# Kernel optimization log

Hardware: AMD Instinct MI355X
Metric: run time of the kernel (lower is better)

## Reference

```python
import jax, jax.numpy as jnp
import numpy as np

D = 1024

def setup_inputs() -> dict:
    key = jax.random.key(0)
    ks = jax.random.split(key, 9)
    s = 1.0 / np.sqrt(D)
    x = jax.random.normal(ks[0], (8, 4096, D), dtype=jnp.float32)
    Wq = jax.random.uniform(ks[1], (D, D), jnp.float32, -s, s)
    bq = jax.random.uniform(ks[2], (D,), jnp.float32, -s, s)
    Wk = jax.random.uniform(ks[3], (D, D), jnp.float32, -s, s)
    bk = jax.random.uniform(ks[4], (D,), jnp.float32, -s, s)
    Wv = jax.random.uniform(ks[5], (D, D), jnp.float32, -s, s)
    bv = jax.random.uniform(ks[6], (D,), jnp.float32, -s, s)
    Wo = jax.random.uniform(ks[7], (D, D), jnp.float32, -s, s)
    bo = jax.random.uniform(ks[8], (D,), jnp.float32, -s, s)
    return {"x": x, "Wq": Wq, "bq": bq, "Wk": Wk, "bk": bk,
            "Wv": Wv, "bv": bv, "Wo": Wo, "bo": bo}

def reference(x, Wq, bq, Wk, bk, Wv, bv, Wo, bo):
    # Linear projections (torch Linear: x @ W.T + b)
    Q = x @ Wq.T + bq
    K = x @ Wk.T + bk
    V = x @ Wv.T + bv
    # elu+1 feature map (positive features)
    Q = jax.nn.elu(Q) + 1.0
    K = jax.nn.elu(K) + 1.0
    # KV outer-product accumulation over sequence: [b, d, e]
    KV = jnp.einsum('bnd,bne->bde', K, V)
    # normalizer Z: [b, n]
    Z = jnp.einsum('bnd,bd->bn', Q, K.sum(axis=1) + 1e-6)
    context = jnp.einsum('bnd,bde->bne', Q, KV) / Z[..., None]
    return context @ Wo.T + bo
```

## Files before the change

kernel.cpp:

```cpp
#include <hip/hip_runtime.h>
#include <stdint.h>

typedef unsigned short u16;
typedef __attribute__((ext_vector_type(8))) short short8;
typedef __attribute__((ext_vector_type(4))) float f32x4;

#define SEQ    4096
#define NB     8
#define DMODEL 1024
#define MTOT   (NB*SEQ)

static __device__ __forceinline__ float bf2f(u16 u){
  union { float f; uint32_t i; } v; v.i = ((uint32_t)u) << 16; return v.f;
}
static __device__ __forceinline__ u16 f2bf(float f){
  union { float f; uint32_t i; } v; v.f = f;
  uint32_t i = v.i + 0x7FFFu + ((v.i >> 16) & 1u);
  return (u16)(i >> 16);
}

static __device__ __forceinline__ void stage16(const void* g, void* l){
  __builtin_amdgcn_global_load_lds(
      (const __attribute__((address_space(1))) void*)g,
      (__attribute__((address_space(3))) void*)l,
      16, 0, 0);
}

__global__ void cvt_f32_bf16(const float* __restrict__ s, u16* __restrict__ d, int n){
  int i = (blockIdx.x * 256 + threadIdx.x) * 8;
  if (i >= n) return;
  float4 a = *(const float4*)(s + i);
  float4 b = *(const float4*)(s + i + 4);
  union { u16 h[8]; short8 v; } o;
  o.h[0]=f2bf(a.x); o.h[1]=f2bf(a.y); o.h[2]=f2bf(a.z); o.h[3]=f2bf(a.w);
  o.h[4]=f2bf(b.x); o.h[5]=f2bf(b.y); o.h[6]=f2bf(b.z); o.h[7]=f2bf(b.w);
  *(short8*)(d + i) = o.v;
}

__global__ __launch_bounds__(256)
void cvt_tr(const float* __restrict__ in, u16* __restrict__ outN,
            u16* __restrict__ outT, int R, int C)
{
  __shared__ float t[64][65];
  const int tid = threadIdx.x;
  const int ntc = C >> 6;
  const int tr = blockIdx.x / ntc, tc = blockIdx.x % ntc;
  const int r0 = tr << 6, c0 = tc << 6;
  const int lrow = tid >> 4, lc4 = (tid & 15) << 2;
  #pragma unroll
  for (int p = 0; p < 4; p++){
    float4 v = *(const float4*)(in + (size_t)(r0 + p*16 + lrow) * C + c0 + lc4);
    t[p*16 + lrow][lc4+0] = v.x; t[p*16 + lrow][lc4+1] = v.y;
    t[p*16 + lrow][lc4+2] = v.z; t[p*16 + lrow][lc4+3] = v.w;
  }
  __syncthreads();
  const int wrow = tid >> 3, wc8 = (tid & 7) << 3;
  if (outN){
    #pragma unroll
    for (int p = 0; p < 2; p++){
      int r = p*32 + wrow;
      union { u16 h[8]; short8 v; } o;
      #pragma unroll
      for (int j = 0; j < 8; j++) o.h[j] = f2bf(t[r][wc8 + j]);
      *(short8*)(outN + (size_t)(r0 + r) * C + c0 + wc8) = o.v;
    }
  }
  #pragma unroll
  for (int p = 0; p < 2; p++){
    int c = p*32 + wrow;
    union { u16 h[8]; short8 v; } o;
    #pragma unroll
    for (int j = 0; j < 8; j++) o.h[j] = f2bf(t[wc8 + j][c]);
    *(short8*)(outT + (size_t)(c0 + c) * R + r0 + wc8) = o.v;
  }
}

__global__ void bo2_kernel(const float* __restrict__ Wo, const float* __restrict__ bv,
                           const float* __restrict__ bo, float* __restrict__ bo2){
  int o = blockIdx.x * 4 + (threadIdx.x >> 6);
  int lane = threadIdx.x & 63;
  const float* row = Wo + (size_t)o * DMODEL;
  float s = 0.f;
  #pragma unroll
  for (int j = 0; j < 4; j++){
    float4 w = *(const float4*)(row + j*256 + lane*4);
    float4 b = *(const float4*)(bv  + j*256 + lane*4);
    s += w.x*b.x + w.y*b.y + w.z*b.z + w.w*b.w;
  }
  for (int off = 32; off; off >>= 1) s += __shfl_xor(s, off);
  if (lane == 0) bo2[o] = bo[o] + s;
}

__global__ void ksum_kernel(const u16* __restrict__ Kt, float* __restrict__ Ksum){
  int wid  = blockIdx.x * 4 + (threadIdx.x >> 6);
  int lane = threadIdx.x & 63;
  int d = wid & 1023, b = wid >> 10;
  const u16* row = Kt + (size_t)d * MTOT + (size_t)b * SEQ;
  float s = 0.f;
  #pragma unroll
  for (int j = 0; j < 8; j++){
    short8 v = *(const short8*)(row + j * 512 + lane * 8);
    #pragma unroll
    for (int t = 0; t < 8; t++) s += bf2f((u16)v[t]);
  }
  for (int off = 32; off; off >>= 1) s += __shfl_xor(s, off);
  if (lane == 0) Ksum[wid] = s + 1e-6f;
}

__global__ void z_kernel(const u16* __restrict__ Qb, const float* __restrict__ Ksum,
                         float* __restrict__ Z){
  int n    = blockIdx.x * 4 + (threadIdx.x >> 6);
  int lane = threadIdx.x & 63;
  const u16*   qrow = Qb + (size_t)n * DMODEL;
  const float* ks   = Ksum + (size_t)(n >> 12) * DMODEL;
  float s = 0.f;
  #pragma unroll
  for (int j = 0; j < 2; j++){
    int base = j * 512 + lane * 8;
    short8 q  = *(const short8*)(qrow + base);
    float4 k0 = *(const float4*)(ks + base);
    float4 k1 = *(const float4*)(ks + base + 4);
    s += bf2f((u16)q[0])*k0.x + bf2f((u16)q[1])*k0.y + bf2f((u16)q[2])*k0.z + bf2f((u16)q[3])*k0.w
       + bf2f((u16)q[4])*k1.x + bf2f((u16)q[5])*k1.y + bf2f((u16)q[6])*k1.z + bf2f((u16)q[7])*k1.w;
  }
  for (int off = 32; off; off >>= 1) s += __shfl_xor(s, off);
  if (lane == 0) Z[n] = s;
}

__global__ __launch_bounds__(256)
void gemm_bt(const u16* __restrict__ A, int ldA,
             const u16* __restrict__ BT, int ldBT, int Kdim,
             u16* __restrict__ Obf, int ldO)
{
  __shared__ u16 Al[128 * 32];
  __shared__ u16 Bl[128 * 32];
  const int tid  = threadIdx.x;
  const int lane = tid & 63;
  const int w    = tid >> 6;
  const int tcol = blockIdx.x;
  const int trow = blockIdx.y;

  const u16* Ap = A  + (size_t)trow * 128 * ldA;
  const u16* Bp = BT + (size_t)tcol * 128 * ldBT;

  f32x4 acc[4][4] = {};
  const int srow = (lane >> 2);
  const int scol = (lane & 3) * 8;

  for (int k0 = 0; k0 < Kdim; k0 += 32){
    #pragma unroll
    for (int i = 0; i < 2; i++){
      int r = w * 32 + i * 16 + srow;
      stage16(Ap + (size_t)r * ldA  + k0 + scol, (char*)Al + w * 2048 + i * 1024);
      stage16(Bp + (size_t)r * ldBT + k0 + scol, (char*)Bl + w * 2048 + i * 1024);
    }
    __syncthreads();
    const int mr = (w >> 1) * 64, nc = (w & 1) * 64;
    const int lr = lane & 15, lk = (lane >> 4) * 8;
    short8 av[4], bv[4];
    #pragma unroll
    for (int mi = 0; mi < 4; mi++) av[mi] = *(const short8*)&Al[(mr + mi*16 + lr)*32 + lk];
    #pragma unroll
    for (int nj = 0; nj < 4; nj++) bv[nj] = *(const short8*)&Bl[(nc + nj*16 + lr)*32 + lk];
    #pragma unroll
    for (int mi = 0; mi < 4; mi++)
      #pragma unroll
      for (int nj = 0; nj < 4; nj++)
        acc[mi][nj] = __builtin_amdgcn_mfma_f32_16x16x32_bf16(av[mi], bv[nj], acc[mi][nj], 0, 0, 0);
    __syncthreads();
  }

  const int mr = (w >> 1) * 64, nc = (w & 1) * 64;
  const int lr = lane & 15, lq = lane >> 4;
  #pragma unroll
  for (int mi = 0; mi < 4; mi++)
    #pragma unroll
    for (int r = 0; r < 4; r++){
      const size_t grow = (size_t)trow * 128 + mr + mi * 16 + lq * 4 + r;
      #pragma unroll
      for (int nj = 0; nj < 4; nj++){
        const size_t gcol = (size_t)tcol * 128 + nc + nj * 16 + lr;
        Obf[grow * ldO + gcol] = f2bf(acc[mi][nj][r]);
      }
    }
}

static __device__ __forceinline__ void stage_chunk(
    const u16* __restrict__ g, int ld, int k0, u16* smem, int baseU16, int tid){
  #pragma unroll
  for (int c = 0; c < 2; c++){
    int lin = c * 512 + tid;
    int row = lin >> 3;
    int slotL = (lin & 7) ^ (row & 7);
    stage16(g + (size_t)row * ld + k0 + slotL * 8,
            (char*)smem + baseU16 * 2 + (c * 8 + (tid >> 6)) * 1024);
  }
}

template<int EPI>
__global__ __launch_bounds__(512, 2)
void gemm8(const u16* __restrict__ A, int ldA,
           const u16* __restrict__ BT, int ldBT, int NT,
           const float* __restrict__ bias, const float* __restrict__ Zv,
           u16* __restrict__ Obf, float* __restrict__ Of32, int ldO)
{
  __shared__ u16 smem[65536];
  const int tid  = threadIdx.x;
  const int lane = tid & 63;
  const int w    = tid >> 6;
  const int wm   = w >> 2, wn = w & 3;
  const int lr   = lane & 15, kq = lane >> 4;

  const int nwg  = gridDim.x;
  const int orig = blockIdx.x;
  const int work = (orig & 7) * (nwg >> 3) + (orig >> 3);
  int trow, tcol; size_t boff = 0;
  if (EPI == 1)      { trow = work & 3; tcol = work >> 2; }
  else               { tcol = work & 3; trow = work >> 2;
                       if (EPI == 2) boff = (size_t)(trow >> 4) * 1024; }
  const int tileM = trow * 256, tileN = tcol * 256;

  const u16* Ag = A + (size_t)tileM * ldA;
  const u16* Bg = BT + boff + (size_t)tileN * ldBT;

  f32x4 acc[8][4] = {};

#define STAGE(buf, k0) do { \
    stage_chunk(Ag,                    ldA,  (k0), smem, (buf) + 0,     tid); \
    stage_chunk(Ag + (size_t)128*ldA,  ldA,  (k0), smem, (buf) + 8192,  tid); \
    stage_chunk(Bg,                    ldBT, (k0), smem, (buf) + 16384, tid); \
    stage_chunk(Bg + (size_t)128*ldBT, ldBT, (k0), smem, (buf) + 24576, tid); \
  } while(0)

#define LDSA(MF, KC) (*(const short8*)(smem + cb + (wm*128 + (MF)*16 + lr)*64 + ((((KC)*4 + kq) ^ (lr & 7)) * 8)))
#define LDSB(NF, KC) (*(const short8*)(smem + cb + 16384 + (wn*64 + (NF)*16 + lr)*64 + ((((KC)*4 + kq) ^ (lr & 7)) * 8)))

  STAGE(0, 0);
  STAGE(32768, 64);
  asm volatile("s_waitcnt vmcnt(8)" ::: "memory");
  __builtin_amdgcn_sched_barrier(0);
  __builtin_amdgcn_s_barrier();

  for (int t = 0; t < NT; t++){
    const int cb = (t & 1) << 15;
    short8 af[4][2], ah[4][2], bf[4][2];
    #pragma unroll
    for (int i = 0; i < 4; i++){ af[i][0] = LDSA(i, 0);   af[i][1] = LDSA(i, 1); }
    #pragma unroll
    for (int i = 0; i < 4; i++){ bf[i][0] = LDSB(i, 0);   bf[i][1] = LDSB(i, 1); }
    __builtin_amdgcn_s_setprio(1);
    #pragma unroll
    for (int mi = 0; mi < 4; mi++)
      #pragma unroll
      for (int nj = 0; nj < 4; nj++)
        #pragma unroll
        for (int kc = 0; kc < 2; kc++)
          acc[mi][nj] = __builtin_amdgcn_mfma_f32_16x16x32_bf16(
              af[mi][kc], bf[nj][kc], acc[mi][nj], 0, 0, 0);
    __builtin_amdgcn_s_setprio(0);
    #pragma unroll
    for (int i = 0; i < 4; i++){ ah[i][0] = LDSA(4+i, 0); ah[i][1] = LDSA(4+i, 1); }
    __builtin_amdgcn_s_setprio(1);
    #pragma unroll
    for (int mi = 0; mi < 4; mi++)
      #pragma unroll
      for (int nj = 0; nj < 4; nj++)
        #pragma unroll
        for (int kc = 0; kc < 2; kc++)
          acc[4+mi][nj] = __builtin_amdgcn_mfma_f32_16x16x32_bf16(
              ah[mi][kc], bf[nj][kc], acc[4+mi][nj], 0, 0, 0);
    __builtin_amdgcn_s_setprio(0);

    __builtin_amdgcn_sched_barrier(0);
    __builtin_amdgcn_s_barrier();
    const int kNN = (t + 2 < NT ? t + 2 : NT - 1) * 64;
    STAGE(cb, kNN);
    asm volatile("s_waitcnt vmcnt(8)" ::: "memory");
    __builtin_amdgcn_sched_barrier(0);
    __builtin_amdgcn_s_barrier();
  }

#undef STAGE
#undef LDSA
#undef LDSB

  #pragma unroll
  for (int mf = 0; mf < 8; mf++){
    #pragma unroll
    for (int r = 0; r < 4; r++){
      const int grow = tileM + wm*128 + mf*16 + kq*4 + r;
      float rowB = 0.f, zin = 0.f;
      if (EPI == 1) rowB = bias[grow];
      if (EPI == 2) zin = 1.f / Zv[grow];
      #pragma unroll
      for (int nf = 0; nf < 4; nf++){
        const int gcol = tileN + wn*64 + nf*16 + lr;
        float v = acc[mf][nf][r];
        if (EPI == 0) { v += bias[gcol]; v = (v > 0.f) ? v + 1.f : __expf(v); }
        if (EPI == 1) { v += rowB;       v = (v > 0.f) ? v + 1.f : __expf(v); }
        if constexpr (EPI == 2) Of32[(size_t)grow * ldO + gcol] = v * zin + bias[gcol];
        else                    Obf [(size_t)grow * ldO + gcol] = f2bf(v);
      }
    }
  }
}

template<int EPI>
__global__ __launch_bounds__(512, 2)
void gemm8h(const u16* __restrict__ A, int ldA,
            const u16* __restrict__ BT, int ldBT, int NT,
            u16* __restrict__ Obf, int ldO)
{
  __shared__ u16 smem[49152];
  const int tid  = threadIdx.x;
  const int lane = tid & 63;
  const int w    = tid >> 6;
  const int wm   = w >> 2, wn = w & 3;
  const int lr   = lane & 15, kq = lane >> 4;

  const int orig = blockIdx.x;
  const int work = (orig & 7) * 32 + (orig >> 3);
  int trow, tcol; size_t aoff = 0, boff = 0, ooff = 0;
  if (EPI == 3) { int zb = work >> 5, sub = work & 31;
                  trow = sub & 7; tcol = sub >> 3;
                  aoff = (size_t)zb * SEQ; boff = aoff; ooff = (size_t)zb << 20; }
  else          { trow = work & 7; tcol = work >> 3; }
  const int tileM = trow * 128, tileN = tcol * 256;

  const u16* Ag = A  + aoff + (size_t)tileM * ldA;
  const u16* Bg = BT + boff + (size_t)tileN * ldBT;

  f32x4 acc[4][4] = {};

#define STAGEH(buf, k0) do { \
    stage_chunk(Ag,                    ldA,  (k0), smem, (buf) + 0,     tid); \
    stage_chunk(Bg,                    ldBT, (k0), smem, (buf) + 8192,  tid); \
    stage_chunk(Bg + (size_t)128*ldBT, ldBT, (k0), smem, (buf) + 16384, tid); \
  } while(0)

#define LDSAH(MF, KC) (*(const short8*)(smem + cb + (wm*64 + (MF)*16 + lr)*64 + ((((KC)*4 + kq) ^ (lr & 7)) * 8)))
#define LDSBH(NF, KC) (*(const short8*)(smem + cb + 8192 + (wn*64 + (NF)*16 + lr)*64 + ((((KC)*4 + kq) ^ (lr & 7)) * 8)))

  STAGEH(0, 0);
  STAGEH(24576, 64);
  asm volatile("s_waitcnt vmcnt(6)" ::: "memory");
  __builtin_amdgcn_sched_barrier(0);
  __builtin_amdgcn_s_barrier();

  for (int t = 0; t < NT; t++){
    const int cb = (t & 1) * 24576;
    short8 af[4][2], bf[4][2];
    #pragma unroll
    for (int i = 0; i < 4; i++){ af[i][0] = LDSAH(i, 0); af[i][1] = LDSAH(i, 1); }
    #pragma unroll
    for (int i = 0; i < 4; i++){ bf[i][0] = LDSBH(i, 0); bf[i][1] = LDSBH(i, 1); }
    __builtin_amdgcn_s_setprio(1);
    #pragma unroll
    for (int mi = 0; mi < 4; mi++)
      #pragma unroll
      for (int nj = 0; nj < 4; nj++)
        #pragma unroll
        for (int kc = 0; kc < 2; kc++)
          acc[mi][nj] = __builtin_amdgcn_mfma_f32_16x16x32_bf16(
              af[mi][kc], bf[nj][kc], acc[mi][nj], 0, 0, 0);
    __builtin_amdgcn_s_setprio(0);
    __builtin_amdgcn_sched_barrier(0);
    __builtin_amdgcn_s_barrier();
    const int kNN = (t + 2 < NT ? t + 2 : NT - 1) * 64;
    STAGEH(cb, kNN);
    asm volatile("s_waitcnt vmcnt(6)" ::: "memory");
    __builtin_amdgcn_sched_barrier(0);
    __builtin_amdgcn_s_barrier();
  }
#undef STAGEH
#undef LDSAH
#undef LDSBH

  #pragma unroll
  for (int mf = 0; mf < 4; mf++){
    #pragma unroll
    for (int r = 0; r < 4; r++){
      const int grow = tileM + wm*64 + mf*16 + kq*4 + r;
      #pragma unroll
      for (int nf = 0; nf < 4; nf++){
        const int gcol = tileN + wn*64 + nf*16 + lr;
        Obf[ooff + (size_t)grow * ldO + gcol] = f2bf(acc[mf][nf][r]);
      }
    }
  }
}

extern "C" void kernel_launch(void* const* d_in, const int* in_sizes, int n_in,
                              void* d_out, int out_size, void* d_ws, size_t ws_size,
                              hipStream_t stream)
{
  const float* x  = (const float*)d_in[0];
  const float* Wq = (const float*)d_in[1];
  const float* bq = (const float*)d_in[2];
  const float* Wk = (const float*)d_in[3];
  const float* bk = (const float*)d_in[4];
  const float* Wv = (const float*)d_in[5];
  const float* bv = (const float*)d_in[6];
  const float* Wo = (const float*)d_in[7];
  const float* bo = (const float*)d_in[8];
  float* out = (float*)d_out;

  char* ws = (char*)d_ws;
  u16*   xb  = (u16*)(ws + 0);
  u16*   Tt  = (u16*)(ws + 0);
  u16*   Gt  = (u16*)(ws + 16777216);
  u16*   xT  = (u16*)(ws + 67108864);
  u16*   Qb  = (u16*)(ws + 134217728);
  u16*   Kt  = (u16*)(ws + 201326592);
  u16*   Wqb = (u16*)(ws + 268435456);
  u16*   Wkb = (u16*)(ws + 270532608);
  u16*   Wob = (u16*)(ws + 272629760);
  u16*   WvT = (u16*)(ws + 274726912);
  u16*   W2b = (u16*)(ws + 276824064);
  float* Ks  = (float*)(ws + 278921216);
  float* Zp  = (float*)(ws + 278953984);
  float* bo2 = (float*)(ws + 279085056);

  cvt_tr<<<8192, 256, 0, stream>>>(x, xb, xT, MTOT, DMODEL);
  cvt_f32_bf16<<<512, 256, 0, stream>>>(Wq, Wqb, DMODEL * DMODEL);
  cvt_f32_bf16<<<512, 256, 0, stream>>>(Wk, Wkb, DMODEL * DMODEL);
  cvt_f32_bf16<<<512, 256, 0, stream>>>(Wo, Wob, DMODEL * DMODEL);
  cvt_tr<<<256, 256, 0, stream>>>(Wv, (u16*)nullptr, WvT, DMODEL, DMODEL);
  bo2_kernel<<<256, 256, 0, stream>>>(Wo, bv, bo, bo2);
  gemm_bt<<<dim3(8, 8, 1), dim3(256), 0, stream>>>(Wob, 1024, WvT, 1024, 1024,
                                                   W2b, 1024);

  gemm8<0><<<512, 512, 0, stream>>>(xb, 1024, Wqb, 1024, 16, bq, nullptr,
                                    Qb, nullptr, 1024);
  gemm8<1><<<512, 512, 0, stream>>>(Wkb, 1024, xb, 1024, 16, bk, nullptr,
                                    Kt, nullptr, MTOT);
  ksum_kernel<<<2048, 256, 0, stream>>>(Kt, Ks);
  z_kernel<<<8192, 256, 0, stream>>>(Qb, Ks, Zp);
  gemm8h<3><<<256, 512, 0, stream>>>(Kt, MTOT, xT, MTOT, 64, Tt, 1024);
  gemm8h<4><<<256, 512, 0, stream>>>(W2b, 1024, Tt, 1024, 16, Gt, 8192);
  gemm8<2><<<512, 512, 0, stream>>>(Qb, 1024, Gt, 8192, 16, bo2, Zp,
                                    nullptr, out, 1024);
}
```

Baseline: 441.0 us.

## Interleave LDS reads, MFMA quadrants and global staging in the GEMM main loop

The GEMM K-loop is split into four MFMA quadrants, each fed by fresh LDS fragment loads and separated by workgroup barriers. Global-to-LDS staging for the next tile now happens in pieces between quadrants, so memory traffic overlaps with matrix work. Before, all staging ran after the compute block. The change adds more barriers per iteration and drops the sched_barrier fences, which risks extra stalls or the compiler reordering instructions.

```diff
diff --git a/kernel.cpp b/kernel.cpp
--- a/kernel.cpp
+++ b/kernel.cpp
@@ -235,54 +235,62 @@
 #define LDSA(MF, KC) (*(const short8*)(smem + cb + (wm*128 + (MF)*16 + lr)*64 + ((((KC)*4 + kq) ^ (lr & 7)) * 8)))
 #define LDSB(NF, KC) (*(const short8*)(smem + cb + 16384 + (wn*64 + (NF)*16 + lr)*64 + ((((KC)*4 + kq) ^ (lr & 7)) * 8)))
 
+#define QUAD(M0, N0, AV, BV) do { \
+  __builtin_amdgcn_s_setprio(1); \
+  _Pragma("unroll") for (int mi = 0; mi < 4; mi++) \
+    _Pragma("unroll") for (int ni = 0; ni < 2; ni++) \
+      _Pragma("unroll") for (int kc = 0; kc < 2; kc++) \
+        acc[(M0)+mi][(N0)+ni] = __builtin_amdgcn_mfma_f32_16x16x32_bf16( \
+            AV[mi][kc], BV[ni][kc], acc[(M0)+mi][(N0)+ni], 0, 0, 0); \
+  __builtin_amdgcn_s_setprio(0); \
+} while(0)
+
   STAGE(0, 0);
   STAGE(32768, 64);
   asm volatile("s_waitcnt vmcnt(8)" ::: "memory");
-  __builtin_amdgcn_sched_barrier(0);
   __builtin_amdgcn_s_barrier();
 
   for (int t = 0; t < NT; t++){
-    const int cb = (t & 1) << 15;
-    short8 af[4][2], ah[4][2], bf[4][2];
-    #pragma unroll
-    for (int i = 0; i < 4; i++){ af[i][0] = LDSA(i, 0);   af[i][1] = LDSA(i, 1); }
-    #pragma unroll
-    for (int i = 0; i < 4; i++){ bf[i][0] = LDSB(i, 0);   bf[i][1] = LDSB(i, 1); }
-    __builtin_amdgcn_s_setprio(1);
-    #pragma unroll
-    for (int mi = 0; mi < 4; mi++)
-      #pragma unroll
-      for (int nj = 0; nj < 4; nj++)
-        #pragma unroll
-        for (int kc = 0; kc < 2; kc++)
-          acc[mi][nj] = __builtin_amdgcn_mfma_f32_16x16x32_bf16(
-              af[mi][kc], bf[nj][kc], acc[mi][nj], 0, 0, 0);
-    __builtin_amdgcn_s_setprio(0);
-    #pragma unroll
-    for (int i = 0; i < 4; i++){ ah[i][0] = LDSA(4+i, 0); ah[i][1] = LDSA(4+i, 1); }
-    __builtin_amdgcn_s_setprio(1);
-    #pragma unroll
-    for (int mi = 0; mi < 4; mi++)
-      #pragma unroll
-      for (int nj = 0; nj < 4; nj++)
-        #pragma unroll
-        for (int kc = 0; kc < 2; kc++)
-          acc[4+mi][nj] = __builtin_amdgcn_mfma_f32_16x16x32_bf16(
-              ah[mi][kc], bf[nj][kc], acc[4+mi][nj], 0, 0, 0);
-    __builtin_amdgcn_s_setprio(0);
-
-    __builtin_amdgcn_sched_barrier(0);
-    __builtin_amdgcn_s_barrier();
+    const int cb  = (t & 1) << 15;
     const int kNN = (t + 2 < NT ? t + 2 : NT - 1) * 64;
-    STAGE(cb, kNN);
+    short8 a0[4][2], a1[4][2], bl[2][2], bh[2][2];
+
+    #pragma unroll
+    for (int i = 0; i < 4; i++){ a0[i][0] = LDSA(i, 0);   a0[i][1] = LDSA(i, 1); }
+    #pragma unroll
+    for (int i = 0; i < 2; i++){ bl[i][0] = LDSB(i, 0);   bl[i][1] = LDSB(i, 1); }
+    __builtin_amdgcn_s_barrier();
+    asm volatile("s_waitcnt lgkmcnt(0)" ::: "memory");
+    QUAD(0, 0, a0, bl);
+    __builtin_amdgcn_s_barrier();
+
+    #pragma unroll
+    for (int i = 0; i < 2; i++){ bh[i][0] = LDSB(2+i, 0); bh[i][1] = LDSB(2+i, 1); }
+    __builtin_amdgcn_s_barrier();
+    asm volatile("s_waitcnt lgkmcnt(0)" ::: "memory");
+    QUAD(0, 2, a0, bh);
+    __builtin_amdgcn_s_barrier();
+
+    #pragma unroll
+    for (int i = 0; i < 4; i++){ a1[i][0] = LDSA(4+i, 0); a1[i][1] = LDSA(4+i, 1); }
+    stage_chunk(Bg, ldBT, kNN, smem, cb + 16384, tid);
+    __builtin_amdgcn_s_barrier();
+    asm volatile("s_waitcnt lgkmcnt(0)" ::: "memory");
+    QUAD(4, 2, a1, bh);
+    __builtin_amdgcn_s_barrier();
+
+    stage_chunk(Bg + (size_t)128*ldBT, ldBT, kNN, smem, cb + 24576, tid);
+    stage_chunk(Ag,                    ldA,  kNN, smem, cb + 0,     tid);
+    stage_chunk(Ag + (size_t)128*ldA,  ldA,  kNN, smem, cb + 8192,  tid);
+    QUAD(4, 0, a1, bl);
     asm volatile("s_waitcnt vmcnt(8)" ::: "memory");
-    __builtin_amdgcn_sched_barrier(0);
     __builtin_amdgcn_s_barrier();
   }
 
 #undef STAGE
 #undef LDSA
 #undef LDSB
+#undef QUAD
 
   #pragma unroll
   for (int mf = 0; mf < 8; mf++){
```

Measured after the change: 428.7 us. 2.8% less time.
